# Performance work log

Hardware: AMD Instinct MI355X
Metric: run time of the kernel (lower is better)

Reference implementation:

```python
import math
import jax, jax.numpy as jnp
import numpy as np

B, S, DM = 2, 1024, 1024
H, D = 16, 64
BUCKETS, MAX_POS = 256, 512
SPAN = BUCKETS          # pos_ebd_size = position_buckets
SCALE = math.sqrt(D * 3)  # scale_factor = 1 + len([c2p, p2c])
EPS = 1e-7


def _make_log_bucket_position(rel, bucket_size, max_position):
    # numpy, matches make_log_bucket_position exactly (static, shape-derived)
    sign = np.sign(rel)
    mid = bucket_size // 2
    abs_pos = np.where((rel < mid) & (rel > -mid), mid - 1, np.abs(rel))
    log_pos = np.ceil(np.log(abs_pos / mid) / np.log((max_position - 1) / mid) * (mid - 1)) + mid
    return np.where(abs_pos <= mid, rel, (log_pos * sign)).astype(np.int64)


def _build_relative_position(q_size, k_size):
    rel = np.arange(q_size)[:, None] - np.arange(k_size)[None, :]
    return _make_log_bucket_position(rel, BUCKETS, MAX_POS)  # [q, k]


def setup_inputs() -> dict:
    key = jax.random.key(0)
    ks = jax.random.split(key, 12)
    w = lambda k, sh: (jax.random.normal(k, sh, jnp.float32) * 0.02)
    return {
        "hidden_states": jax.random.normal(ks[0], (B, S, DM), jnp.float32),
        "rel_embeddings": jax.random.normal(ks[1], (2 * SPAN, DM), jnp.float32),
        "Wq": w(ks[2], (DM, DM)), "bq": jnp.zeros((DM,), jnp.float32),
        "Wk": w(ks[3], (DM, DM)), "bk": jnp.zeros((DM,), jnp.float32),
        "Wv": w(ks[4], (DM, DM)), "bv": jnp.zeros((DM,), jnp.float32),
        "Wo": w(ks[5], (DM, DM)), "bo": jnp.zeros((DM,), jnp.float32),
        "ln_w": jnp.ones((DM,), jnp.float32), "ln_b": jnp.zeros((DM,), jnp.float32),
        "attention_mask": jnp.ones((B, 1, S, S), jnp.int32),
    }


def reference(hidden_states, rel_embeddings, Wq, bq, Wk, bk, Wv, bv, Wo, bo, ln_w, ln_b, attention_mask):
    b, s, _ = hidden_states.shape
    heads = lambda x: x.reshape(b, s, H, D).transpose(0, 2, 1, 3)  # [B,H,S,D]
    q = heads(hidden_states @ Wq + bq)
    k = heads(hidden_states @ Wk + bk)
    v = heads(hidden_states @ Wv + bv)

    # content-to-content scores
    scores = jnp.einsum('bhqd,bhkd->bhqk', q, k) / SCALE

    # disentangled relative-position bias (share_att_key=True: reuse key/query proj)
    rel = _build_relative_position(s, s)                      # [S,S] static int
    c2p_idx = np.clip(rel + SPAN, 0, 2 * SPAN - 1)            # [S,S]
    p2c_idx = np.clip(-rel + SPAN, 0, 2 * SPAN - 1)           # [S,S]
    pos_k = (rel_embeddings @ Wk + bk).reshape(2 * SPAN, H, D).transpose(1, 0, 2)  # [H,P,D]
    pos_q = (rel_embeddings @ Wq + bq).reshape(2 * SPAN, H, D).transpose(1, 0, 2)  # [H,P,D]

    qi = np.arange(s)[:, None]  # row index for gather along bucket axis
    c2p = jnp.einsum('bhqd,hpd->bhqp', q, pos_k)              # [B,H,S,2K]
    scores = scores + c2p[:, :, qi, c2p_idx] / SCALE          # gather -> [B,H,S,S]
    p2c = jnp.einsum('bhkd,hpd->bhkp', k, pos_q)              # [B,H,S,2K]
    scores = scores + jnp.swapaxes(p2c[:, :, qi, p2c_idx], -1, -2) / SCALE

    # XSoftmax: masked softmax, masked positions zeroed
    m = attention_mask.astype(bool)
    probs = jax.nn.softmax(jnp.where(m, scores, -jnp.inf), axis=-1)
    probs = jnp.where(m, probs, 0.0)

    ctx = jnp.einsum('bhqk,bhkd->bhqd', probs, v).transpose(0, 2, 1, 3).reshape(b, s, H * D)

    # DebertaV2SelfOutput: dense + (eval-mode dropout = identity) + LayerNorm residual
    h = ctx @ Wo + bo + hidden_states
    mu = h.mean(-1, keepdims=True)
    var = ((h - mu) ** 2).mean(-1, keepdims=True)
    return (h - mu) * jax.lax.rsqrt(var + EPS) * ln_w + ln_b
```

## Files before the change

### kernel.cpp

```cpp
#include <hip/hip_runtime.h>
#include <hip/hip_bf16.h>

#define Sv   1024
#define DMv  1024
#define Hv   16
#define PBv  512
#define INVSCALE 0.07216878364870322f

typedef unsigned short u16;
typedef unsigned int   u32;
typedef short  short8  __attribute__((ext_vector_type(8)));
typedef float  float4v __attribute__((ext_vector_type(4)));

__device__ __forceinline__ float b2f(u16 u) {
    union { u32 u; float f; } c; c.u = ((u32)u) << 16; return c.f;
}
__device__ __forceinline__ u16 f2b(float f) {
    union { float f; u32 u; } c; c.f = f;
    u32 u = c.u;
    return (u16)((u + 0x7fffu + ((u >> 16) & 1u)) >> 16);
}
__device__ __forceinline__ float ldE(const void* p, size_t i, bool f32) {
    return f32 ? ((const float*)p)[i] : b2f(((const u16*)p)[i]);
}

__global__ void setup_kernel(const u32* __restrict__ w, int* __restrict__ flag,
                             int* __restrict__ tbl) {
    if (blockIdx.x == 0) {
        int t = threadIdx.x;
        if (t < 64) {
            int c = 0;
            #pragma unroll
            for (int i = 0; i < 4; i++) {
                u32 v = w[t * 4 + i];
                c += (((v >> 23) & 0xFFu) < 0x80u) ? 1 : 0;
            }
            #pragma unroll
            for (int off = 32; off > 0; off >>= 1) c += __shfl_down(c, off, 64);
            if (t == 0) *flag = (c > 128) ? 1 : 0;
        }
        return;
    }
    int i = (blockIdx.x - 1) * 256 + threadIdx.x;
    if (i >= 2047) return;
    int rel = i - 1023;
    const int mid = 128;
    int abs_pos = (rel < mid && rel > -mid) ? (mid - 1) : (rel < 0 ? -rel : rel);
    int bucket;
    if (abs_pos <= mid) {
        bucket = rel;
    } else {
        double lp = ceil(log((double)abs_pos / 128.0) / log(511.0 / 128.0) * 127.0) + 128.0;
        bucket = (int)lp * (rel > 0 ? 1 : -1);
    }
    int idx = bucket + 256;
    idx = idx < 0 ? 0 : (idx > 511 ? 511 : idx);
    tbl[i] = idx;
}

__global__ __launch_bounds__(256) void cvt2_kernel(
    const void* __restrict__ s0, u16* __restrict__ d0,
    const void* __restrict__ s1, u16* __restrict__ d1,
    const int* __restrict__ flagp)
{
    bool f32 = (*flagp != 0);
    const void* src; u16* dst; size_t i;
    if (blockIdx.x < 1024) {
        src = s0; dst = d0;
        i = ((size_t)blockIdx.x * 256 + threadIdx.x) * 8;
    } else {
        src = s1; dst = d1;
        i = ((size_t)(blockIdx.x - 1024) * 256 + threadIdx.x) * 8;
    }
    if (f32) {
        const float* s = (const float*)src + i;
        float4 a = *(const float4*)s;
        float4 b = *(const float4*)(s + 4);
        uint4 o = make_uint4(f2b(a.x) | (f2b(a.y) << 16), f2b(a.z) | (f2b(a.w) << 16),
                             f2b(b.x) | (f2b(b.y) << 16), f2b(b.z) | (f2b(b.w) << 16));
        *(uint4*)(dst + i) = o;
    } else {
        *(uint4*)(dst + i) = *(const uint4*)((const u16*)src + i);
    }
}

__global__ __launch_bounds__(256) void transpose_cvt(
    const void* __restrict__ S0, const void* __restrict__ S1,
    const void* __restrict__ S2, u16* __restrict__ out,
    const int* __restrict__ flagp)
{
    bool f32 = (*flagp != 0);
    int z = blockIdx.z;
    const void* S = (z == 0) ? S0 : (z == 1) ? S1 : S2;
    u16* O = out + (size_t)z * 1048576;
    int k0 = blockIdx.x * 64, n0 = blockIdx.y * 64;
    __shared__ u16 Ls[64][72];
    int t = threadIdx.x;
    int r = t >> 2, cseg = (t & 3) * 16;

    u16 v[16];
    size_t base = (size_t)(k0 + r) * 1024 + n0 + cseg;
    if (f32) {
        const float* p = (const float*)S + base;
        #pragma unroll
        for (int i = 0; i < 16; i += 4) {
            float4 f = *(const float4*)(p + i);
            v[i] = f2b(f.x); v[i + 1] = f2b(f.y); v[i + 2] = f2b(f.z); v[i + 3] = f2b(f.w);
        }
    } else {
        const u16* p = (const u16*)S + base;
        uint4 a = *(const uint4*)p, b = *(const uint4*)(p + 8);
        u32 wd[8] = {a.x, a.y, a.z, a.w, b.x, b.y, b.z, b.w};
        #pragma unroll
        for (int i = 0; i < 8; i++) { v[2 * i] = (u16)(wd[i] & 0xffff); v[2 * i + 1] = (u16)(wd[i] >> 16); }
    }
    #pragma unroll
    for (int i = 0; i < 16; i++) Ls[cseg + i][r] = v[i];
    __syncthreads();

    int n = t >> 2, kseg = (t & 3) * 16;
    u16* op = O + (size_t)(n0 + n) * 1024 + k0 + kseg;
    *(uint4*)op       = *(const uint4*)&Ls[n][kseg];
    *(uint4*)(op + 8) = *(const uint4*)&Ls[n][kseg + 8];
}

__global__ __launch_bounds__(256) void wgemm_bt(
    const u16* __restrict__ A,
    const u16* __restrict__ B0, const u16* __restrict__ B1, const u16* __restrict__ B2,
    const void* __restrict__ b0, const void* __restrict__ b1, const void* __restrict__ b2,
    u16* __restrict__ O0, u16* __restrict__ O1, u16* __restrict__ O2,
    const int* __restrict__ flagp, int vseg, int sseg)
{
    bool f32 = (*flagp != 0);
    __shared__ u16 As[128][72];
    __shared__ u16 Bs[128][72];

    int t = threadIdx.x;
    int seg = blockIdx.x >> 3;
    int n0  = (blockIdx.x & 7) * 128;
    int m0  = blockIdx.y * 128;
    const u16* Bt = (seg == 0) ? B0 : (seg == 1) ? B1 : B2;
    const void* bi = (seg == 0) ? b0 : (seg == 1) ? b1 : b2;
    u16* O = (seg == 0) ? O0 : (seg == 1) ? O1 : O2;
    float es = (seg == sseg) ? INVSCALE : 1.0f;

    int w = t >> 6, lane = t & 63;
    int quad = lane >> 4, l16 = lane & 15;
    int wm = (w >> 1) * 64, wn = (w & 1) * 64;

    float4v acc[4][4];
    #pragma unroll
    for (int i = 0; i < 4; i++)
        #pragma unroll
        for (int j = 0; j < 4; j++)
            acc[i][j] = (float4v){0.f, 0.f, 0.f, 0.f};

    int sam = t >> 1, sak = (t & 1) * 32;

    for (int k0 = 0; k0 < 1024; k0 += 64) {
        const u16* ap = A  + (size_t)(m0 + sam) * 1024 + k0 + sak;
        const u16* bp = Bt + (size_t)(n0 + sam) * 1024 + k0 + sak;
        uint4 a0 = *(const uint4*)(ap + 0),  a1 = *(const uint4*)(ap + 8);
        uint4 a2 = *(const uint4*)(ap + 16), a3 = *(const uint4*)(ap + 24);
        uint4 q0 = *(const uint4*)(bp + 0),  q1 = *(const uint4*)(bp + 8);
        uint4 q2 = *(const uint4*)(bp + 16), q3 = *(const uint4*)(bp + 24);
        __syncthreads();
        *(uint4*)&As[sam][sak + 0]  = a0;
        *(uint4*)&As[sam][sak + 8]  = a1;
        *(uint4*)&As[sam][sak + 16] = a2;
        *(uint4*)&As[sam][sak + 24] = a3;
        *(uint4*)&Bs[sam][sak + 0]  = q0;
        *(uint4*)&Bs[sam][sak + 8]  = q1;
        *(uint4*)&Bs[sam][sak + 16] = q2;
        *(uint4*)&Bs[sam][sak + 24] = q3;
        __syncthreads();

        #pragma unroll
        for (int kk = 0; kk < 64; kk += 32) {
            short8 af[4], bf[4];
            #pragma unroll
            for (int i = 0; i < 4; i++)
                af[i] = *(const short8*)&As[wm + i * 16 + l16][kk + quad * 8];
            #pragma unroll
            for (int j = 0; j < 4; j++)
                bf[j] = *(const short8*)&Bs[wn + j * 16 + l16][kk + quad * 8];
            #pragma unroll
            for (int j = 0; j < 4; j++)
                #pragma unroll
                for (int i = 0; i < 4; i++)
                    acc[i][j] = __builtin_amdgcn_mfma_f32_16x16x32_bf16(af[i], bf[j], acc[i][j], 0, 0, 0);
        }
    }

    if (seg == vseg) {
        #pragma unroll
        for (int j = 0; j < 4; j++) {
            int ncol = n0 + wn + j * 16 + l16;
            float bv = ldE(bi, ncol, f32);
            u16* obase = O + (size_t)(ncol >> 6) * 131072 + (size_t)(ncol & 63) * 2048;
            #pragma unroll
            for (int i = 0; i < 4; i++) {
                int rbase = m0 + wm + i * 16 + quad * 4;
                u32 w0 = (u32)f2b((acc[i][j][0] + bv) * es) | ((u32)f2b((acc[i][j][1] + bv) * es) << 16);
                u32 w1 = (u32)f2b((acc[i][j][2] + bv) * es) | ((u32)f2b((acc[i][j][3] + bv) * es) << 16);
                *(uint2*)(obase + rbase) = make_uint2(w0, w1);
            }
        }
    } else {
        #pragma unroll
        for (int j = 0; j < 4; j++) {
            int ncol = n0 + wn + j * 16 + l16;
            float bv = ldE(bi, ncol, f32);
            #pragma unroll
            for (int i = 0; i < 4; i++) {
                int rbase = m0 + wm + i * 16 + quad * 4;
                #pragma unroll
                for (int r = 0; r < 4; r++)
                    O[(size_t)(rbase + r) * 1024 + ncol] = f2b((acc[i][j][r] + bv) * es);
            }
        }
    }
}

__global__ __launch_bounds__(256) void wgemm_bt_m64(
    const u16* __restrict__ A, const u16* __restrict__ Bt,
    const void* __restrict__ bi, u16* __restrict__ O,
    const int* __restrict__ flagp)
{
    bool f32 = (*flagp != 0);
    __shared__ u16 As[64][72];
    __shared__ u16 Bs[128][72];

    int t = threadIdx.x;
    int n0 = blockIdx.x * 128;
    int m0 = blockIdx.y * 64;

    int w = t >> 6, lane = t & 63;
    int quad = lane >> 4, l16 = lane & 15;
    int wm = (w >> 1) * 32, wn = (w & 1) * 64;

    float4v acc[2][4];
    #pragma unroll
    for (int i = 0; i < 2; i++)
        #pragma unroll
        for (int j = 0; j < 4; j++)
            acc[i][j] = (float4v){0.f, 0.f, 0.f, 0.f};

    int ra = t >> 2, ka = (t & 3) * 16;
    int rb = t >> 1, kb = (t & 1) * 32;

    for (int k0 = 0; k0 < 1024; k0 += 64) {
        const u16* ap = A  + (size_t)(m0 + ra) * 1024 + k0 + ka;
        const u16* bp = Bt + (size_t)(n0 + rb) * 1024 + k0 + kb;
        uint4 a0 = *(const uint4*)(ap + 0), a1 = *(const uint4*)(ap + 8);
        uint4 q0 = *(const uint4*)(bp + 0),  q1 = *(const uint4*)(bp + 8);
        uint4 q2 = *(const uint4*)(bp + 16), q3 = *(const uint4*)(bp + 24);
        __syncthreads();
        *(uint4*)&As[ra][ka + 0] = a0;
        *(uint4*)&As[ra][ka + 8] = a1;
        *(uint4*)&Bs[rb][kb + 0]  = q0;
        *(uint4*)&Bs[rb][kb + 8]  = q1;
        *(uint4*)&Bs[rb][kb + 16] = q2;
        *(uint4*)&Bs[rb][kb + 24] = q3;
        __syncthreads();

        #pragma unroll
        for (int kk = 0; kk < 64; kk += 32) {
            short8 af[2], bf[4];
            #pragma unroll
            for (int i = 0; i < 2; i++)
                af[i] = *(const short8*)&As[wm + i * 16 + l16][kk + quad * 8];
            #pragma unroll
            for (int j = 0; j < 4; j++)
                bf[j] = *(const short8*)&Bs[wn + j * 16 + l16][kk + quad * 8];
            #pragma unroll
            for (int j = 0; j < 4; j++)
                #pragma unroll
                for (int i = 0; i < 2; i++)
                    acc[i][j] = __builtin_amdgcn_mfma_f32_16x16x32_bf16(af[i], bf[j], acc[i][j], 0, 0, 0);
        }
    }

    #pragma unroll
    for (int j = 0; j < 4; j++) {
        int ncol = n0 + wn + j * 16 + l16;
        float bv = ldE(bi, ncol, f32);
        #pragma unroll
        for (int i = 0; i < 2; i++) {
            int rbase = m0 + wm + i * 16 + quad * 4;
            #pragma unroll
            for (int r = 0; r < 4; r++)
                O[(size_t)(rbase + r) * 1024 + ncol] = f2b(acc[i][j][r] + bv);
        }
    }
}

__global__ __launch_bounds__(256) void pos_score_mfma(
    const u16* __restrict__ Xq, const u16* __restrict__ Xk,
    const u16* __restrict__ PK, const u16* __restrict__ PQ,
    u16* __restrict__ outq, u16* __restrict__ outk)
{
    int zT = blockIdx.z;
    const u16* X = zT ? Xk : Xq;
    const u16* P = zT ? PQ : PK;
    u16* out     = zT ? outk : outq;

    __shared__ u16 As[128][72];
    __shared__ u16 Bs[128][72];
    int t = threadIdx.x;
    int h  = blockIdx.x >> 2;
    int j0 = (blockIdx.x & 3) * 128;
    int m0 = blockIdx.y * 128;

    int w = t >> 6, lane = t & 63;
    int quad = lane >> 4, l16 = lane & 15;
    int wm = (w >> 1) * 64, wn = (w & 1) * 64;

    int sam = t >> 1, sak = (t & 1) * 32;
    {
        const u16* xp = X + (size_t)(m0 + sam) * 1024 + h * 64 + sak;
        *(uint4*)&As[sam][sak +  0] = *(const uint4*)(xp +  0);
        *(uint4*)&As[sam][sak +  8] = *(const uint4*)(xp +  8);
        *(uint4*)&As[sam][sak + 16] = *(const uint4*)(xp + 16);
        *(uint4*)&As[sam][sak + 24] = *(const uint4*)(xp + 24);
        const u16* pp = P + (size_t)(j0 + sam) * 1024 + h * 64 + sak;
        *(uint4*)&Bs[sam][sak +  0] = *(const uint4*)(pp +  0);
        *(uint4*)&Bs[sam][sak +  8] = *(const uint4*)(pp +  8);
        *(uint4*)&Bs[sam][sak + 16] = *(const uint4*)(pp + 16);
        *(uint4*)&Bs[sam][sak + 24] = *(const uint4*)(pp + 24);
    }
    __syncthreads();

    float4v acc[4][4];
    #pragma unroll
    for (int i = 0; i < 4; i++)
        #pragma unroll
        for (int j = 0; j < 4; j++)
            acc[i][j] = (float4v){0.f, 0.f, 0.f, 0.f};

    #pragma unroll
    for (int k0 = 0; k0 < 64; k0 += 32) {
        short8 af[4], bf[4];
        #pragma unroll
        for (int i = 0; i < 4; i++)
            af[i] = *(const short8*)&As[wm + i * 16 + l16][k0 + quad * 8];
        #pragma unroll
        for (int j = 0; j < 4; j++)
            bf[j] = *(const short8*)&Bs[wn + j * 16 + l16][k0 + quad * 8];
        #pragma unroll
        for (int j = 0; j < 4; j++)
            #pragma unroll
            for (int i = 0; i < 4; i++)
                acc[i][j] = __builtin_amdgcn_mfma_f32_16x16x32_bf16(af[i], bf[j], acc[i][j], 0, 0, 0);
    }

    if (zT == 0) {
        #pragma unroll
        for (int j = 0; j < 4; j++) {
            int jc = j0 + wn + j * 16 + l16;
            #pragma unroll
            for (int i = 0; i < 4; i++) {
                int rbase = m0 + wm + i * 16 + quad * 4;
                #pragma unroll
                for (int r = 0; r < 4; r++)
                    out[((size_t)h * Sv + rbase + r) * PBv + jc] = f2b(acc[i][j][r]);
            }
        }
    } else {
        #pragma unroll
        for (int j = 0; j < 4; j++) {
            int jc = j0 + wn + j * 16 + l16;
            u16* obase = out + (size_t)h * (PBv * Sv) + (size_t)jc * Sv;
            #pragma unroll
            for (int i = 0; i < 4; i++) {
                int rbase = m0 + wm + i * 16 + quad * 4;
                u32 w0 = (u32)f2b(acc[i][j][0]) | ((u32)f2b(acc[i][j][1]) << 16);
                u32 w1 = (u32)f2b(acc[i][j][2]) | ((u32)f2b(acc[i][j][3]) << 16);
                *(uint2*)(obase + rbase) = make_uint2(w0, w1);
            }
        }
    }
}

__global__ __launch_bounds__(256, 2) void attn6_kernel(
    const u16* __restrict__ Q, const u16* __restrict__ K,
    const u16* __restrict__ Vtg,
    const u16* __restrict__ C2P,
    const u16* __restrict__ P2Ct,
    const int* __restrict__ tbl, u16* __restrict__ CTX)
{
    __shared__ u16 Qc[32][72];
    __shared__ u16 Kc[2][64][72];
    __shared__ u16 Vc[2][64][72];
    __shared__ u16 Pb[4][16][72];
    __shared__ short stbl[2047];
    __shared__ float msh[2][2][16], lsh[2][2][16];

    int t = threadIdx.x, w = t >> 6, lane = t & 63;
    int qg = w >> 1, ks = w & 1;
    int quad = lane >> 4, l16 = lane & 15;
    int h = blockIdx.y, q0 = blockIdx.x * 32;

    for (int i = t; i < 2047; i += 256) stbl[i] = (short)tbl[i];
    {
        int row = t >> 3, dseg = (t & 7) * 8;
        *(uint4*)&Qc[row][dseg] =
            *(const uint4*)(Q + (size_t)(q0 + row) * DMv + h * 64 + dseg);
    }
    __syncthreads();

    short8 afq0 = *(const short8*)&Qc[qg * 16 + l16][quad * 8];
    short8 afq1 = *(const short8*)&Qc[qg * 16 + l16][quad * 8 + 32];

    int qrow = q0 + qg * 16 + quad * 4;
    const u16* c2p_h  = C2P  + (size_t)h * (Sv * PBv);
    const u16* p2ct_h = P2Ct + (size_t)h * (PBv * Sv);
    const u16* vt_h   = Vtg  + (size_t)h * 131072;

    float m[4] = {-1e30f, -1e30f, -1e30f, -1e30f};
    float l[4] = {0.f, 0.f, 0.f, 0.f};
    float4v Ov[4];
    #pragma unroll
    for (int j = 0; j < 4; j++) Ov[j] = (float4v){0.f, 0.f, 0.f, 0.f};

    int srow = (t >> 1) & 63, sseg = (t & 1) * 32, ssp = t >> 7;

    for (int c = 0; c < 8; c++) {
        __syncthreads();
        {
            int kglob = ssp * 512 + c * 64 + srow;
            const u16* kp = K + (size_t)kglob * DMv + h * 64 + sseg;
            uint4 a0 = *(const uint4*)(kp + 0);
            uint4 a1 = *(const uint4*)(kp + 8);
            uint4 a2 = *(const uint4*)(kp + 16);
            uint4 a3 = *(const uint4*)(kp + 24);
            *(uint4*)&Kc[ssp][srow][sseg + 0]  = a0;
            *(uint4*)&Kc[ssp][srow][sseg + 8]  = a1;
            *(uint4*)&Kc[ssp][srow][sseg + 16] = a2;
            *(uint4*)&Kc[ssp][srow][sseg + 24] = a3;
            const u16* vp = vt_h + (size_t)srow * 2048 + ssp * 512 + c * 64 + sseg;
            uint4 v0 = *(const uint4*)(vp + 0);
            uint4 v1 = *(const uint4*)(vp + 8);
            uint4 v2 = *(const uint4*)(vp + 16);
            uint4 v3 = *(const uint4*)(vp + 24);
            *(uint4*)&Vc[ssp][srow][sseg + 0]  = v0;
            *(uint4*)&Vc[ssp][srow][sseg + 8]  = v1;
            *(uint4*)&Vc[ssp][srow][sseg + 16] = v2;
            *(uint4*)&Vc[ssp][srow][sseg + 24] = v3;
        }
        __syncthreads();

        int kb = ks * 512 + c * 64;
        float p[4][4];
        #pragma unroll
        for (int j = 0; j < 4; j++) {
            short8 bk0 = *(const short8*)&Kc[ks][j * 16 + l16][quad * 8];
            short8 bk1 = *(const short8*)&Kc[ks][j * 16 + l16][quad * 8 + 32];
            float4v a = (float4v){0.f, 0.f, 0.f, 0.f};
            a = __builtin_amdgcn_mfma_f32_16x16x32_bf16(afq0, bk0, a, 0, 0, 0);
            a = __builtin_amdgcn_mfma_f32_16x16x32_bf16(afq1, bk1, a, 0, 0, 0);
            #pragma unroll
            for (int r = 0; r < 4; r++) p[j][r] = a[r];
        }
        #pragma unroll
        for (int j = 0; j < 4; j++) {
            int k = kb + j * 16 + l16;
            #pragma unroll
            for (int r = 0; r < 4; r++) {
                int q = qrow + r;
                int idx = stbl[q - k + 1023];
                p[j][r] = p[j][r] + b2f(c2p_h[(size_t)q * PBv + idx])
                                  + b2f(p2ct_h[(size_t)idx * Sv + k]);
            }
        }
        float corr[4];
        #pragma unroll
        for (int r = 0; r < 4; r++) {
            float v = fmaxf(fmaxf(p[0][r], p[1][r]), fmaxf(p[2][r], p[3][r]));
            v = fmaxf(v, __shfl_xor(v, 1, 64));
            v = fmaxf(v, __shfl_xor(v, 2, 64));
            v = fmaxf(v, __shfl_xor(v, 4, 64));
            v = fmaxf(v, __shfl_xor(v, 8, 64));
            float nm = fmaxf(m[r], v);
            corr[r] = __expf(m[r] - nm);
            m[r] = nm;
        }
        #pragma unroll
        for (int r = 0; r < 4; r++) {
            #pragma unroll
            for (int j = 0; j < 4; j++) p[j][r] = __expf(p[j][r] - m[r]);
            float s = p[0][r] + p[1][r] + p[2][r] + p[3][r];
            s += __shfl_xor(s, 1, 64);
            s += __shfl_xor(s, 2, 64);
            s += __shfl_xor(s, 4, 64);
            s += __shfl_xor(s, 8, 64);
            l[r] = l[r] * corr[r] + s;
            #pragma unroll
            for (int j = 0; j < 4; j++) Ov[j][r] *= corr[r];
        }
        #pragma unroll
        for (int j = 0; j < 4; j++)
            #pragma unroll
            for (int r = 0; r < 4; r++)
                Pb[w][quad * 4 + r][j * 16 + l16] = f2b(p[j][r]);
        short8 ap0 = *(const short8*)&Pb[w][l16][quad * 8];
        short8 ap1 = *(const short8*)&Pb[w][l16][quad * 8 + 32];
        #pragma unroll
        for (int j = 0; j < 4; j++) {
            short8 bv0 = *(const short8*)&Vc[ks][j * 16 + l16][quad * 8];
            short8 bv1 = *(const short8*)&Vc[ks][j * 16 + l16][quad * 8 + 32];
            Ov[j] = __builtin_amdgcn_mfma_f32_16x16x32_bf16(ap0, bv0, Ov[j], 0, 0, 0);
            Ov[j] = __builtin_amdgcn_mfma_f32_16x16x32_bf16(ap1, bv1, Ov[j], 0, 0, 0);
        }
    }

    if (l16 == 0) {
        #pragma unroll
        for (int r = 0; r < 4; r++) {
            msh[qg][ks][quad * 4 + r] = m[r];
            lsh[qg][ks][quad * 4 + r] = l[r];
        }
    }
    __syncthreads();
    float scl[4];
    #pragma unroll
    for (int r = 0; r < 4; r++) {
        int row = quad * 4 + r;
        float m0 = msh[qg][0][row], m1 = msh[qg][1][row];
        float M = fmaxf(m0, m1);
        float L = lsh[qg][0][row] * __expf(m0 - M) + lsh[qg][1][row] * __expf(m1 - M);
        scl[r] = __expf(m[r] - M) / L;
    }
    float* Obuf = (float*)&Kc[0][0][0];
    if (ks == 1) {
        #pragma unroll
        for (int j = 0; j < 4; j++)
            #pragma unroll
            for (int r = 0; r < 4; r++)
                Obuf[(qg * 16 + quad * 4 + r) * 66 + j * 16 + l16] = Ov[j][r] * scl[r];
    }
    __syncthreads();
    if (ks == 0) {
        #pragma unroll
        for (int j = 0; j < 4; j++)
            #pragma unroll
            for (int r = 0; r < 4; r++) {
                float v = Ov[j][r] * scl[r]
                        + Obuf[(qg * 16 + quad * 4 + r) * 66 + j * 16 + l16];
                CTX[(size_t)(qrow + r) * DMv + h * 64 + j * 16 + l16] = f2b(v);
            }
    }
}

__global__ __launch_bounds__(256) void ln_kernel(
    const u16* __restrict__ Hb, const void* __restrict__ hidden,
    const void* __restrict__ lnw, const void* __restrict__ lnb,
    void* __restrict__ out, const int* __restrict__ flagp)
{
    bool f32 = (*flagp != 0);
    int row = blockIdx.x;
    int t = threadIdx.x;
    const u16* hp = Hb + (size_t)row * DMv;

    uint2 hv = *(const uint2*)(hp + t * 4);
    float x[4];
    x[0] = b2f(hv.x & 0xffff); x[1] = b2f(hv.x >> 16);
    x[2] = b2f(hv.y & 0xffff); x[3] = b2f(hv.y >> 16);
    size_t rb = (size_t)row * DMv + t * 4;
    if (f32) {
        float4 xv = *(const float4*)((const float*)hidden + rb);
        x[0] += xv.x; x[1] += xv.y; x[2] += xv.z; x[3] += xv.w;
    } else {
        uint2 xv = *(const uint2*)((const u16*)hidden + rb);
        x[0] += b2f(xv.x & 0xffff); x[1] += b2f(xv.x >> 16);
        x[2] += b2f(xv.y & 0xffff); x[3] += b2f(xv.y >> 16);
    }

    float s1 = x[0] + x[1] + x[2] + x[3];
    float s2 = x[0] * x[0] + x[1] * x[1] + x[2] * x[2] + x[3] * x[3];
    #pragma unroll
    for (int off = 32; off > 0; off >>= 1) {
        s1 += __shfl_down(s1, off, 64);
        s2 += __shfl_down(s2, off, 64);
    }
    __shared__ float r1[4], r2[4];
    int wave = t >> 6, lane = t & 63;
    if (lane == 0) { r1[wave] = s1; r2[wave] = s2; }
    __syncthreads();
    float ts1 = r1[0] + r1[1] + r1[2] + r1[3];
    float ts2 = r2[0] + r2[1] + r2[2] + r2[3];
    float mu  = ts1 * (1.0f / DMv);
    float var = fmaxf(ts2 * (1.0f / DMv) - mu * mu, 0.f);
    float rs  = rsqrtf(var + 1e-7f);
    #pragma unroll
    for (int i = 0; i < 4; i++) {
        int c = t * 4 + i;
        float v = (x[i] - mu) * rs * ldE(lnw, c, f32) + ldE(lnb, c, f32);
        if (f32) ((float*)out)[(size_t)row * DMv + c] = v;
        else     ((u16*)out)[(size_t)row * DMv + c] = f2b(v);
    }
}

extern "C" void kernel_launch(void* const* d_in, const int* in_sizes, int n_in,
                              void* d_out, int out_size, void* d_ws, size_t ws_size,
                              hipStream_t stream) {
    const void* hidden = d_in[0];
    const void* rel    = d_in[1];
    const void* Wq = d_in[2];  const void* bq = d_in[3];
    const void* Wk = d_in[4];  const void* bk = d_in[5];
    const void* Wv = d_in[6];  const void* bv = d_in[7];
    const void* Wo = d_in[8];  const void* bo = d_in[9];
    const void* lnw = d_in[10]; const void* lnb = d_in[11];

    const size_t MB = 1u << 20;
    char* ws = (char*)d_ws;
    int* FLAG = (int*)ws;
    int* TBL  = (int*)(ws + 1024);
    char* base = ws + (64 << 10);
    u16* Qb   = (u16*)(base + 0 * MB);
    u16* Kb   = (u16*)(base + 4 * MB);
    u16* Vt   = (u16*)(base + 8 * MB);
    u16* CTX  = (u16*)(base + 12 * MB);
    u16* Xb   = (u16*)(base + 12 * MB);
    u16* PKb  = (u16*)(base + 16 * MB);
    u16* PQb  = (u16*)(base + 17 * MB);
    u16* HB   = (u16*)(base + 16 * MB);
    u16* C2P  = (u16*)(base + 18 * MB);
    u16* WoT  = (u16*)(base + 20 * MB);
    u16* P2Ct = (u16*)(base + 34 * MB);
    u16* WqT  = (u16*)(base + 34 * MB);
    u16* WkT  = (u16*)(base + 36 * MB);
    u16* WvT  = (u16*)(base + 38 * MB);
    u16* relb = (u16*)(base + 40 * MB);

    dim3 blk(256);

    setup_kernel<<<9, blk, 0, stream>>>((const u32*)Wq, FLAG, TBL);
    cvt2_kernel<<<1280, blk, 0, stream>>>(hidden, Xb, rel, relb, FLAG);
    transpose_cvt<<<dim3(16, 16, 3), blk, 0, stream>>>(Wq, Wk, Wv, WqT, FLAG);

    wgemm_bt<<<dim3(24, 16), blk, 0, stream>>>(
        Xb, WqT, WkT, WvT, bq, bk, bv, Qb, Kb, Vt, FLAG, 2, 0);
    wgemm_bt<<<dim3(16, 4), blk, 0, stream>>>(
        relb, WkT, WqT, nullptr, bk, bq, nullptr, PKb, PQb, nullptr, FLAG, -1, 1);

    for (int b = 0; b < 2; b++) {
        size_t off = (size_t)b * Sv * DMv;
        pos_score_mfma<<<dim3(64, 8, 2), blk, 0, stream>>>(
            Qb + off, Kb + off, PKb, PQb, C2P, P2Ct);
        attn6_kernel<<<dim3(32, 16), blk, 0, stream>>>(
            Qb + off, Kb + off, Vt + (size_t)b * 1024, C2P, P2Ct, TBL, CTX + off);
    }

    transpose_cvt<<<dim3(16, 16, 1), blk, 0, stream>>>(Wo, nullptr, nullptr, WoT, FLAG);
    wgemm_bt_m64<<<dim3(8, 32), blk, 0, stream>>>(CTX, WoT, bo, HB, FLAG);
    ln_kernel<<<2048, blk, 0, stream>>>(HB, hidden, lnw, lnb, d_out, FLAG);
}
```

Baseline: 287.2 us.

## Merge projection GEMMs, batch attention launches, and raise attention occupancy

The QKV and position-embedding projections are merged into one 64x128-tile GEMM launch of 896 blocks. The Wo transpose joins the Q/K/V transpose launch. The per-batch loop over pos_score and attention becomes single launches with the batch on grid z, which needs a larger workspace so both batches' C2P/P2C buffers live at once. The attention kernel reuses one shared buffer for Q and P tiles and shrinks the bucket table to raise occupancy from 2 to 3 blocks per CU, cutting launch count and tail effects at the cost of more memory footprint.

```diff
diff --git a/kernel.cpp b/kernel.cpp
--- a/kernel.cpp
+++ b/kernel.cpp
@@ -86,12 +86,12 @@
 
 __global__ __launch_bounds__(256) void transpose_cvt(
     const void* __restrict__ S0, const void* __restrict__ S1,
-    const void* __restrict__ S2, u16* __restrict__ out,
-    const int* __restrict__ flagp)
+    const void* __restrict__ S2, const void* __restrict__ S3,
+    u16* __restrict__ out, const int* __restrict__ flagp)
 {
     bool f32 = (*flagp != 0);
     int z = blockIdx.z;
-    const void* S = (z == 0) ? S0 : (z == 1) ? S1 : S2;
+    const void* S = (z == 0) ? S0 : (z == 1) ? S1 : (z == 2) ? S2 : S3;
     u16* O = out + (size_t)z * 1048576;
     int k0 = blockIdx.x * 64, n0 = blockIdx.y * 64;
     __shared__ u16 Ls[64][72];
@@ -124,117 +124,32 @@
     *(uint4*)(op + 8) = *(const uint4*)&Ls[n][kseg + 8];
 }
 
-__global__ __launch_bounds__(256) void wgemm_bt(
-    const u16* __restrict__ A,
-    const u16* __restrict__ B0, const u16* __restrict__ B1, const u16* __restrict__ B2,
-    const void* __restrict__ b0, const void* __restrict__ b1, const void* __restrict__ b2,
-    u16* __restrict__ O0, u16* __restrict__ O1, u16* __restrict__ O2,
-    const int* __restrict__ flagp, int vseg, int sseg)
-{
-    bool f32 = (*flagp != 0);
-    __shared__ u16 As[128][72];
-    __shared__ u16 Bs[128][72];
-
-    int t = threadIdx.x;
-    int seg = blockIdx.x >> 3;
-    int n0  = (blockIdx.x & 7) * 128;
-    int m0  = blockIdx.y * 128;
-    const u16* Bt = (seg == 0) ? B0 : (seg == 1) ? B1 : B2;
-    const void* bi = (seg == 0) ? b0 : (seg == 1) ? b1 : b2;
-    u16* O = (seg == 0) ? O0 : (seg == 1) ? O1 : O2;
-    float es = (seg == sseg) ? INVSCALE : 1.0f;
-
-    int w = t >> 6, lane = t & 63;
-    int quad = lane >> 4, l16 = lane & 15;
-    int wm = (w >> 1) * 64, wn = (w & 1) * 64;
-
-    float4v acc[4][4];
-    #pragma unroll
-    for (int i = 0; i < 4; i++)
-        #pragma unroll
-        for (int j = 0; j < 4; j++)
-            acc[i][j] = (float4v){0.f, 0.f, 0.f, 0.f};
-
-    int sam = t >> 1, sak = (t & 1) * 32;
-
-    for (int k0 = 0; k0 < 1024; k0 += 64) {
-        const u16* ap = A  + (size_t)(m0 + sam) * 1024 + k0 + sak;
-        const u16* bp = Bt + (size_t)(n0 + sam) * 1024 + k0 + sak;
-        uint4 a0 = *(const uint4*)(ap + 0),  a1 = *(const uint4*)(ap + 8);
-        uint4 a2 = *(const uint4*)(ap + 16), a3 = *(const uint4*)(ap + 24);
-        uint4 q0 = *(const uint4*)(bp + 0),  q1 = *(const uint4*)(bp + 8);
-        uint4 q2 = *(const uint4*)(bp + 16), q3 = *(const uint4*)(bp + 24);
-        __syncthreads();
-        *(uint4*)&As[sam][sak + 0]  = a0;
-        *(uint4*)&As[sam][sak + 8]  = a1;
-        *(uint4*)&As[sam][sak + 16] = a2;
-        *(uint4*)&As[sam][sak + 24] = a3;
-        *(uint4*)&Bs[sam][sak + 0]  = q0;
-        *(uint4*)&Bs[sam][sak + 8]  = q1;
-        *(uint4*)&Bs[sam][sak + 16] = q2;
-        *(uint4*)&Bs[sam][sak + 24] = q3;
-        __syncthreads();
-
-        #pragma unroll
-        for (int kk = 0; kk < 64; kk += 32) {
-            short8 af[4], bf[4];
-            #pragma unroll
-            for (int i = 0; i < 4; i++)
-                af[i] = *(const short8*)&As[wm + i * 16 + l16][kk + quad * 8];
-            #pragma unroll
-            for (int j = 0; j < 4; j++)
-                bf[j] = *(const short8*)&Bs[wn + j * 16 + l16][kk + quad * 8];
-            #pragma unroll
-            for (int j = 0; j < 4; j++)
-                #pragma unroll
-                for (int i = 0; i < 4; i++)
-                    acc[i][j] = __builtin_amdgcn_mfma_f32_16x16x32_bf16(af[i], bf[j], acc[i][j], 0, 0, 0);
-        }
-    }
-
-    if (seg == vseg) {
-        #pragma unroll
-        for (int j = 0; j < 4; j++) {
-            int ncol = n0 + wn + j * 16 + l16;
-            float bv = ldE(bi, ncol, f32);
-            u16* obase = O + (size_t)(ncol >> 6) * 131072 + (size_t)(ncol & 63) * 2048;
-            #pragma unroll
-            for (int i = 0; i < 4; i++) {
-                int rbase = m0 + wm + i * 16 + quad * 4;
-                u32 w0 = (u32)f2b((acc[i][j][0] + bv) * es) | ((u32)f2b((acc[i][j][1] + bv) * es) << 16);
-                u32 w1 = (u32)f2b((acc[i][j][2] + bv) * es) | ((u32)f2b((acc[i][j][3] + bv) * es) << 16);
-                *(uint2*)(obase + rbase) = make_uint2(w0, w1);
-            }
-        }
-    } else {
-        #pragma unroll
-        for (int j = 0; j < 4; j++) {
-            int ncol = n0 + wn + j * 16 + l16;
-            float bv = ldE(bi, ncol, f32);
-            #pragma unroll
-            for (int i = 0; i < 4; i++) {
-                int rbase = m0 + wm + i * 16 + quad * 4;
-                #pragma unroll
-                for (int r = 0; r < 4; r++)
-                    O[(size_t)(rbase + r) * 1024 + ncol] = f2b((acc[i][j][r] + bv) * es);
-            }
-        }
-    }
-}
-
-__global__ __launch_bounds__(256) void wgemm_bt_m64(
-    const u16* __restrict__ A, const u16* __restrict__ Bt,
-    const void* __restrict__ bi, u16* __restrict__ O,
+__global__ __launch_bounds__(256) void gemm5_kernel(
+    const u16* __restrict__ Xb, const u16* __restrict__ relb,
+    const u16* __restrict__ WqT, const u16* __restrict__ WkT, const u16* __restrict__ WvT,
+    const void* __restrict__ bq, const void* __restrict__ bk, const void* __restrict__ bv,
+    u16* __restrict__ Qb, u16* __restrict__ Kb, u16* __restrict__ Vt,
+    u16* __restrict__ PKb, u16* __restrict__ PQb,
     const int* __restrict__ flagp)
 {
     bool f32 = (*flagp != 0);
     __shared__ u16 As[64][72];
     __shared__ u16 Bs[128][72];
 
+    int x = blockIdx.x;
+    int seg, mtile, ntile;
+    if (x < 768) { seg = x >> 8; int rem = x & 255; ntile = rem & 7; mtile = rem >> 3; }
+    else         { int y = x - 768; seg = 3 + (y >> 6); int rem = y & 63; ntile = rem & 7; mtile = rem >> 3; }
+
+    const u16* A  = (seg < 3) ? Xb : relb;
+    const u16* Bt = (seg == 0 || seg == 4) ? WqT : (seg == 2 ? WvT : WkT);
+    const void* bi = (seg == 0 || seg == 4) ? bq : (seg == 2 ? bv : bk);
+    u16* O = (seg == 0) ? Qb : (seg == 1) ? Kb : (seg == 2) ? Vt : (seg == 3) ? PKb : PQb;
+    float es = (seg == 0 || seg == 4) ? INVSCALE : 1.0f;
+    bool vstore = (seg == 2);
+
+    int n0 = ntile * 128, m0 = mtile * 64;
     int t = threadIdx.x;
-    int n0 = blockIdx.x * 128;
-    int m0 = blockIdx.y * 64;
-
     int w = t >> 6, lane = t & 63;
     int quad = lane >> 4, l16 = lane & 15;
     int wm = (w >> 1) * 32, wn = (w & 1) * 64;
@@ -281,6 +196,95 @@
         }
     }
 
+    if (vstore) {
+        #pragma unroll
+        for (int j = 0; j < 4; j++) {
+            int ncol = n0 + wn + j * 16 + l16;
+            float bv = ldE(bi, ncol, f32);
+            u16* obase = O + (size_t)(ncol >> 6) * 131072 + (size_t)(ncol & 63) * 2048;
+            #pragma unroll
+            for (int i = 0; i < 2; i++) {
+                int rbase = m0 + wm + i * 16 + quad * 4;
+                u32 w0 = (u32)f2b(acc[i][j][0] + bv) | ((u32)f2b(acc[i][j][1] + bv) << 16);
+                u32 w1 = (u32)f2b(acc[i][j][2] + bv) | ((u32)f2b(acc[i][j][3] + bv) << 16);
+                *(uint2*)(obase + rbase) = make_uint2(w0, w1);
+            }
+        }
+    } else {
+        #pragma unroll
+        for (int j = 0; j < 4; j++) {
+            int ncol = n0 + wn + j * 16 + l16;
+            float bv = ldE(bi, ncol, f32);
+            #pragma unroll
+            for (int i = 0; i < 2; i++) {
+                int rbase = m0 + wm + i * 16 + quad * 4;
+                #pragma unroll
+                for (int r = 0; r < 4; r++)
+                    O[(size_t)(rbase + r) * 1024 + ncol] = f2b((acc[i][j][r] + bv) * es);
+            }
+        }
+    }
+}
+
+__global__ __launch_bounds__(256) void wgemm_bt_m64(
+    const u16* __restrict__ A, const u16* __restrict__ Bt,
+    const void* __restrict__ bi, u16* __restrict__ O,
+    const int* __restrict__ flagp)
+{
+    bool f32 = (*flagp != 0);
+    __shared__ u16 As[64][72];
+    __shared__ u16 Bs[128][72];
+
+    int t = threadIdx.x;
+    int n0 = blockIdx.x * 128;
+    int m0 = blockIdx.y * 64;
+
+    int w = t >> 6, lane = t & 63;
+    int quad = lane >> 4, l16 = lane & 15;
+    int wm = (w >> 1) * 32, wn = (w & 1) * 64;
+
+    float4v acc[2][4];
+    #pragma unroll
+    for (int i = 0; i < 2; i++)
+        #pragma unroll
+        for (int j = 0; j < 4; j++)
+            acc[i][j] = (float4v){0.f, 0.f, 0.f, 0.f};
+
+    int ra = t >> 2, ka = (t & 3) * 16;
+    int rb = t >> 1, kb = (t & 1) * 32;
+
+    for (int k0 = 0; k0 < 1024; k0 += 64) {
+        const u16* ap = A  + (size_t)(m0 + ra) * 1024 + k0 + ka;
+        const u16* bp = Bt + (size_t)(n0 + rb) * 1024 + k0 + kb;
+        uint4 a0 = *(const uint4*)(ap + 0), a1 = *(const uint4*)(ap + 8);
+        uint4 q0 = *(const uint4*)(bp + 0),  q1 = *(const uint4*)(bp + 8);
+        uint4 q2 = *(const uint4*)(bp + 16), q3 = *(const uint4*)(bp + 24);
+        __syncthreads();
+        *(uint4*)&As[ra][ka + 0] = a0;
+        *(uint4*)&As[ra][ka + 8] = a1;
+        *(uint4*)&Bs[rb][kb + 0]  = q0;
+        *(uint4*)&Bs[rb][kb + 8]  = q1;
+        *(uint4*)&Bs[rb][kb + 16] = q2;
+        *(uint4*)&Bs[rb][kb + 24] = q3;
+        __syncthreads();
+
+        #pragma unroll
+        for (int kk = 0; kk < 64; kk += 32) {
+            short8 af[2], bf[4];
+            #pragma unroll
+            for (int i = 0; i < 2; i++)
+                af[i] = *(const short8*)&As[wm + i * 16 + l16][kk + quad * 8];
+            #pragma unroll
+            for (int j = 0; j < 4; j++)
+                bf[j] = *(const short8*)&Bs[wn + j * 16 + l16][kk + quad * 8];
+            #pragma unroll
+            for (int j = 0; j < 4; j++)
+                #pragma unroll
+                for (int i = 0; i < 2; i++)
+                    acc[i][j] = __builtin_amdgcn_mfma_f32_16x16x32_bf16(af[i], bf[j], acc[i][j], 0, 0, 0);
+        }
+    }
+
     #pragma unroll
     for (int j = 0; j < 4; j++) {
         int ncol = n0 + wn + j * 16 + l16;
@@ -296,14 +300,15 @@
 }
 
 __global__ __launch_bounds__(256) void pos_score_mfma(
-    const u16* __restrict__ Xq, const u16* __restrict__ Xk,
+    const u16* __restrict__ Qb, const u16* __restrict__ Kb,
     const u16* __restrict__ PK, const u16* __restrict__ PQ,
-    u16* __restrict__ outq, u16* __restrict__ outk)
+    u16* __restrict__ C2P, u16* __restrict__ P2Ct)
 {
-    int zT = blockIdx.z;
-    const u16* X = zT ? Xk : Xq;
+    int z = blockIdx.z;
+    int bb = z >> 1, zT = z & 1;
+    const u16* X = (zT ? Kb : Qb) + (size_t)bb * (Sv * DMv);
     const u16* P = zT ? PQ : PK;
-    u16* out     = zT ? outk : outq;
+    u16* out     = (zT ? P2Ct : C2P) + (size_t)bb * ((size_t)Hv * Sv * PBv);
 
     __shared__ u16 As[128][72];
     __shared__ u16 Bs[128][72];
@@ -382,40 +387,45 @@
     }
 }
 
-__global__ __launch_bounds__(256, 2) void attn6_kernel(
-    const u16* __restrict__ Q, const u16* __restrict__ K,
+__global__ __launch_bounds__(256, 3) void attn8_kernel(
+    const u16* __restrict__ Qg, const u16* __restrict__ Kg,
     const u16* __restrict__ Vtg,
-    const u16* __restrict__ C2P,
-    const u16* __restrict__ P2Ct,
-    const int* __restrict__ tbl, u16* __restrict__ CTX)
+    const u16* __restrict__ C2Pg,
+    const u16* __restrict__ P2Ctg,
+    const int* __restrict__ tbl, u16* __restrict__ CTXg)
 {
-    __shared__ u16 Qc[32][72];
     __shared__ u16 Kc[2][64][72];
     __shared__ u16 Vc[2][64][72];
-    __shared__ u16 Pb[4][16][72];
-    __shared__ short stbl[2047];
+    __shared__ u16 qp[4608];
+    __shared__ short stbl[1056];
     __shared__ float msh[2][2][16], lsh[2][2][16];
 
     int t = threadIdx.x, w = t >> 6, lane = t & 63;
     int qg = w >> 1, ks = w & 1;
     int quad = lane >> 4, l16 = lane & 15;
     int h = blockIdx.y, q0 = blockIdx.x * 32;
-
-    for (int i = t; i < 2047; i += 256) stbl[i] = (short)tbl[i];
+    int bz = blockIdx.z;
+
+    const u16* Q   = Qg + (size_t)bz * (Sv * DMv);
+    const u16* K   = Kg + (size_t)bz * (Sv * DMv);
+    u16* CTX       = CTXg + (size_t)bz * (Sv * DMv);
+    const u16* c2p_h  = C2Pg  + (size_t)bz * ((size_t)Hv * Sv * PBv) + (size_t)h * (Sv * PBv);
+    const u16* p2ct_h = P2Ctg + (size_t)bz * ((size_t)Hv * PBv * Sv) + (size_t)h * (PBv * Sv);
+    const u16* vt_h   = Vtg + (size_t)h * 131072 + bz * 1024;
+
+    for (int i = t; i < 1055; i += 256) stbl[i] = (short)tbl[q0 + i];
     {
         int row = t >> 3, dseg = (t & 7) * 8;
-        *(uint4*)&Qc[row][dseg] =
+        *(uint4*)&qp[row * 72 + dseg] =
             *(const uint4*)(Q + (size_t)(q0 + row) * DMv + h * 64 + dseg);
     }
     __syncthreads();
 
-    short8 afq0 = *(const short8*)&Qc[qg * 16 + l16][quad * 8];
-    short8 afq1 = *(const short8*)&Qc[qg * 16 + l16][quad * 8 + 32];
+    short8 afq0 = *(const short8*)&qp[(qg * 16 + l16) * 72 + quad * 8];
+    short8 afq1 = *(const short8*)&qp[(qg * 16 + l16) * 72 + quad * 8 + 32];
 
     int qrow = q0 + qg * 16 + quad * 4;
-    const u16* c2p_h  = C2P  + (size_t)h * (Sv * PBv);
-    const u16* p2ct_h = P2Ct + (size_t)h * (PBv * Sv);
-    const u16* vt_h   = Vtg  + (size_t)h * 131072;
+    int lbase = qg * 16 + quad * 4 + 1023;
 
     float m[4] = {-1e30f, -1e30f, -1e30f, -1e30f};
     float l[4] = {0.f, 0.f, 0.f, 0.f};
@@ -468,7 +478,7 @@
             #pragma unroll
             for (int r = 0; r < 4; r++) {
                 int q = qrow + r;
-                int idx = stbl[q - k + 1023];
+                int idx = stbl[lbase + r - k];
                 p[j][r] = p[j][r] + b2f(c2p_h[(size_t)q * PBv + idx])
                                   + b2f(p2ct_h[(size_t)idx * Sv + k]);
             }
@@ -502,9 +512,9 @@
         for (int j = 0; j < 4; j++)
             #pragma unroll
             for (int r = 0; r < 4; r++)
-                Pb[w][quad * 4 + r][j * 16 + l16] = f2b(p[j][r]);
-        short8 ap0 = *(const short8*)&Pb[w][l16][quad * 8];
-        short8 ap1 = *(const short8*)&Pb[w][l16][quad * 8 + 32];
+                qp[(w * 16 + quad * 4 + r) * 72 + j * 16 + l16] = f2b(p[j][r]);
+        short8 ap0 = *(const short8*)&qp[(w * 16 + l16) * 72 + quad * 8];
+        short8 ap1 = *(const short8*)&qp[(w * 16 + l16) * 72 + quad * 8 + 32];
         #pragma unroll
         for (int j = 0; j < 4; j++) {
             short8 bv0 = *(const short8*)&Vc[ks][j * 16 + l16][quad * 8];
@@ -617,42 +627,34 @@
     int* FLAG = (int*)ws;
     int* TBL  = (int*)(ws + 1024);
     char* base = ws + (64 << 10);
-    u16* Qb   = (u16*)(base + 0 * MB);
-    u16* Kb   = (u16*)(base + 4 * MB);
-    u16* Vt   = (u16*)(base + 8 * MB);
+    u16* Qb   = (u16*)(base +  0 * MB);
+    u16* Kb   = (u16*)(base +  4 * MB);
+    u16* Vt   = (u16*)(base +  8 * MB);
     u16* CTX  = (u16*)(base + 12 * MB);
-    u16* Xb   = (u16*)(base + 12 * MB);
     u16* PKb  = (u16*)(base + 16 * MB);
     u16* PQb  = (u16*)(base + 17 * MB);
-    u16* HB   = (u16*)(base + 16 * MB);
-    u16* C2P  = (u16*)(base + 18 * MB);
-    u16* WoT  = (u16*)(base + 20 * MB);
-    u16* P2Ct = (u16*)(base + 34 * MB);
-    u16* WqT  = (u16*)(base + 34 * MB);
-    u16* WkT  = (u16*)(base + 36 * MB);
-    u16* WvT  = (u16*)(base + 38 * MB);
-    u16* relb = (u16*)(base + 40 * MB);
+    u16* HB   = (u16*)(base + 18 * MB);
+    u16* C2P  = (u16*)(base + 22 * MB);
+    u16* P2Ct = (u16*)(base + 54 * MB);
+    u16* WqT  = (u16*)(base + 86 * MB);
+    u16* WkT  = (u16*)(base + 88 * MB);
+    u16* WvT  = (u16*)(base + 90 * MB);
+    u16* WoT  = (u16*)(base + 92 * MB);
+    u16* relb = (u16*)(base + 94 * MB);
+    u16* Xb   = (u16*)(base + 96 * MB);
 
     dim3 blk(256);
 
     setup_kernel<<<9, blk, 0, stream>>>((const u32*)Wq, FLAG, TBL);
     cvt2_kernel<<<1280, blk, 0, stream>>>(hidden, Xb, rel, relb, FLAG);
-    transpose_cvt<<<dim3(16, 16, 3), blk, 0, stream>>>(Wq, Wk, Wv, WqT, FLAG);
-
-    wgemm_bt<<<dim3(24, 16), blk, 0, stream>>>(
-        Xb, WqT, WkT, WvT, bq, bk, bv, Qb, Kb, Vt, FLAG, 2, 0);
-    wgemm_bt<<<dim3(16, 4), blk, 0, stream>>>(
-        relb, WkT, WqT, nullptr, bk, bq, nullptr, PKb, PQb, nullptr, FLAG, -1, 1);
-
-    for (int b = 0; b < 2; b++) {
-        size_t off = (size_t)b * Sv * DMv;
-        pos_score_mfma<<<dim3(64, 8, 2), blk, 0, stream>>>(
-            Qb + off, Kb + off, PKb, PQb, C2P, P2Ct);
-        attn6_kernel<<<dim3(32, 16), blk, 0, stream>>>(
-            Qb + off, Kb + off, Vt + (size_t)b * 1024, C2P, P2Ct, TBL, CTX + off);
-    }
-
-    transpose_cvt<<<dim3(16, 16, 1), blk, 0, stream>>>(Wo, nullptr, nullptr, WoT, FLAG);
+    transpose_cvt<<<dim3(16, 16, 4), blk, 0, stream>>>(Wq, Wk, Wv, Wo, WqT, FLAG);
+
+    gemm5_kernel<<<896, blk, 0, stream>>>(
+        Xb, relb, WqT, WkT, WvT, bq, bk, bv, Qb, Kb, Vt, PKb, PQb, FLAG);
+
+    pos_score_mfma<<<dim3(64, 8, 4), blk, 0, stream>>>(Qb, Kb, PKb, PQb, C2P, P2Ct);
+    attn8_kernel<<<dim3(32, 16, 2), blk, 0, stream>>>(Qb, Kb, Vt, C2P, P2Ct, TBL, CTX);
+
     wgemm_bt_m64<<<dim3(8, 32), blk, 0, stream>>>(CTX, WoT, bo, HB, FLAG);
     ln_kernel<<<2048, blk, 0, stream>>>(HB, hidden, lnw, lnb, d_out, FLAG);
 }
```

After: 323.3 us. 1.13x slower.
